# Optimization experiments

Hardware: AMD Instinct MI355X
Metric: run time of the kernel (lower is better)

## Reference

```python
import jax, jax.numpy as jnp
import numpy as np

B, NQ, NM, NHR, D, H, FF = 16, 100, 5440, 4096, 256, 8, 2048

def _ln(x, w, b):
    m = x.mean(-1, keepdims=True)
    v = ((x - m) ** 2).mean(-1, keepdims=True)
    return (x - m) * jax.lax.rsqrt(v + 1e-5) * w + b

def setup_inputs():
    key = jax.random.key(0)
    ks = iter(jax.random.split(key, 32))
    def rn(shape, s=1.0):
        return jax.random.normal(next(ks), shape, jnp.float32) * s
    return {
        'tgt': rn((B, NQ, D)),
        'memory': rn((B, NM, D)),
        'memory_hr': rn((B, NHR, D)),
        'prior_attn_bias': rn((B, NQ, NM)),
        'query_pos': rn((B, NQ, D)),
        'ln_cross_w': jnp.ones((D,)), 'ln_cross_b': jnp.zeros((D,)),
        'q_w': rn((D, D), 0.02), 'q_b': jnp.zeros((D,)),
        'k_w': rn((D, D), 0.02), 'k_b': jnp.zeros((D,)),
        'v_w': rn((D, D), 0.02), 'v_b': jnp.zeros((D,)),
        'out_w': rn((D, D), 0.02), 'out_b': jnp.zeros((D,)),
        'ln_self_w': jnp.ones((D,)), 'ln_self_b': jnp.zeros((D,)),
        'sa_in_w': rn((3 * D, D), 0.02), 'sa_in_b': jnp.zeros((3 * D,)),
        'sa_out_w': rn((D, D), 0.02), 'sa_out_b': jnp.zeros((D,)),
        'ln_ffn_w': jnp.ones((D,)), 'ln_ffn_b': jnp.zeros((D,)),
        'lin1_w': rn((FF, D), 0.02), 'lin1_b': jnp.zeros((FF,)),
        'lin2_w': rn((D, FF), 0.02), 'lin2_b': jnp.zeros((D,)),
        'me_w': rn((D, D), 0.02), 'me_b': jnp.zeros((D,)),
    }

def reference(tgt, memory, memory_hr, prior_attn_bias, query_pos,
              ln_cross_w, ln_cross_b, q_w, q_b, k_w, k_b, v_w, v_b,
              out_w, out_b, ln_self_w, ln_self_b, sa_in_w, sa_in_b,
              sa_out_w, sa_out_b, ln_ffn_w, ln_ffn_b, lin1_w, lin1_b,
              lin2_w, lin2_b, me_w, me_b):
    b, nq, d = tgt.shape
    nm = memory.shape[1]
    h = H
    dh = d // h
    scale = dh ** -0.5
    # ---- cross-attention with additive prior bias (eval mode: dropout = id) ----
    x = _ln(tgt, ln_cross_w, ln_cross_b)
    q = ((x + query_pos) @ q_w.T + q_b).reshape(b, nq, h, dh)
    k = (memory @ k_w.T + k_b).reshape(b, nm, h, dh)
    v = (memory @ v_w.T + v_b).reshape(b, nm, h, dh)
    attn = jnp.einsum('bqhd,bmhd->bhqm', q, k) * scale + prior_attn_bias[:, None]  # [b,h,nq,nm]
    a = jax.nn.softmax(attn, axis=-1)
    o = jnp.einsum('bhqm,bmhd->bqhd', a, v).reshape(b, nq, d)
    tgt = tgt + (o @ out_w.T + out_b)
    # ---- self-attention (torch nn.MultiheadAttention, batch_first, eval) ----
    z = _ln(tgt, ln_self_w, ln_self_b)
    zq = z + query_pos
    qs = (zq @ sa_in_w[:d].T + sa_in_b[:d]).reshape(b, nq, h, dh)
    ks = (zq @ sa_in_w[d:2 * d].T + sa_in_b[d:2 * d]).reshape(b, nq, h, dh)
    vs = (z @ sa_in_w[2 * d:].T + sa_in_b[2 * d:]).reshape(b, nq, h, dh)
    sattn = jax.nn.softmax(jnp.einsum('bqhd,bmhd->bhqm', qs, ks) * scale, axis=-1)
    so = jnp.einsum('bhqm,bmhd->bqhd', sattn, vs).reshape(b, nq, d)
    tgt = tgt + (so @ sa_out_w.T + sa_out_b)
    # ---- FFN ----
    y = _ln(tgt, ln_ffn_w, ln_ffn_b)
    y = jax.nn.gelu(y @ lin1_w.T + lin1_b, approximate=False) @ lin2_w.T + lin2_b
    tgt = tgt + y
    # ---- mask branch ----
    mask_logits = jnp.einsum('bqd,bmd->bqm', tgt @ me_w.T + me_b, memory_hr)
    return (tgt, mask_logits)
```

## Files before the change

kernel.cpp:

```cpp
#include <hip/hip_runtime.h>

typedef unsigned short u16;
typedef unsigned int u32;
typedef __bf16 bf16x8 __attribute__((ext_vector_type(8)));
typedef float f32x4 __attribute__((ext_vector_type(4)));
typedef float f32x16 __attribute__((ext_vector_type(16)));

#define NCH 34
#define NSTEP 5

__device__ __forceinline__ u16 f2b(float f) {
  u32 u = __float_as_uint(f);
  u32 r = (u + 0x7fffu + ((u >> 16) & 1u)) >> 16;
  return (u16)r;
}
__device__ __forceinline__ float b2f(u16 h) {
  return __uint_as_float(((u32)h) << 16);
}
__device__ __forceinline__ bf16x8 zero8() {
  union { uint4 u; bf16x8 v; } z; z.u = make_uint4(0u, 0u, 0u, 0u); return z.v;
}
__device__ __forceinline__ u32 cvtpk(float lo, float hi) {
  u32 r;
  asm("v_cvt_pk_bf16_f32 %0, %1, %2" : "=v"(r) : "v"(lo), "v"(hi));
  return r;
}

struct Seg { const float* in; u16* out; int n4; };
struct PrepArgs {
  Seg seg[7];
  const float *k_w, *v_w, *k_b, *v_b, *pbias;
  u16 *Wf;
  uint4 *biasT5;
  float *kvB;
};

__global__ __launch_bounds__(256)
void prep_kernel(PrepArgs a)
{
  __shared__ float S[100][34];
  const int bx = blockIdx.x, tid = threadIdx.x;
  if (bx < 1472) {
    int bxr = bx;
#pragma unroll
    for (int k = 0; k < 7; ++k) {
      const int nb = a.seg[k].n4 >> 8;
      if (bxr < nb) {
        const int i = bxr * 256 + tid;
        const float4 f = *(const float4*)(a.seg[k].in + (size_t)i * 4);
        uint2 pk; pk.x = cvtpk(f.x, f.y); pk.y = cvtpk(f.z, f.w);
        *(uint2*)(a.seg[k].out + (size_t)i * 4) = pk;
        return;
      }
      bxr -= nb;
    }
    return;
  } else if (bx < 1536) {
    const int i = bx - 1472, gI = i >> 3, ks = i & 7;
    const int nt = tid >> 6, lane = tid & 63, lr = lane & 15, g = lane >> 4;
    const float* src = (gI < 4 ? a.k_w + (size_t)(gI * 64 + nt * 16 + lr) * 256
                               : a.v_w + (size_t)((gI - 4) * 64 + nt * 16 + lr) * 256)
                       + ks * 32 + g * 8;
    const float4 f0 = *(const float4*)src;
    const float4 f1 = *(const float4*)(src + 4);
    uint4 pk;
    pk.x = cvtpk(f0.x, f0.y); pk.y = cvtpk(f0.z, f0.w);
    pk.z = cvtpk(f1.x, f1.y); pk.w = cvtpk(f1.z, f1.w);
    *(uint4*)(a.Wf + (size_t)((gI * 8 + ks) * 4 + nt) * 512 + lane * 8) = pk;
  } else if (bx < 1538) {
    const int i = (bx - 1536) * 256 + tid;
    a.kvB[i] = (i < 256) ? a.k_b[i] : a.v_b[i - 256];
  } else {
    const int bt = bx - 1538;
    const int b = bt / 170, sg = bt - b * 170;
    const int m0 = sg * 32;
    for (int idx = tid; idx < 800; idx += 256) {
      const int q = idx >> 3, seg = idx & 7;
      const float4 v = *(const float4*)(a.pbias + (size_t)(b * 100 + q) * 5440 + m0 + seg * 4);
      S[q][seg * 4 + 0] = v.x; S[q][seg * 4 + 1] = v.y;
      S[q][seg * 4 + 2] = v.z; S[q][seg * 4 + 3] = v.w;
    }
    __syncthreads();
#pragma unroll
    for (int pass = 0; pass < 2; ++pass) {
      const int idx = pass * 256 + tid;
      const int qb = idx >> 7, r2 = idx & 127;
      const int half = r2 >> 6, lane = r2 & 63;
      const int q = qb * 32 + (lane & 31), hh = lane >> 5;
      u16 hv[8];
#pragma unroll
      for (int i = 0; i < 8; ++i) {
        const int reg = half * 8 + i;
        const int m = (reg & 3) + 8 * (reg >> 2) + 4 * hh;
        hv[i] = (q < 100) ? f2b(S[q][m]) : (u16)0;
      }
      uint4 pk;
      pk.x = (u32)hv[0] | ((u32)hv[1] << 16);
      pk.y = (u32)hv[2] | ((u32)hv[3] << 16);
      pk.z = (u32)hv[4] | ((u32)hv[5] << 16);
      pk.w = (u32)hv[6] | ((u32)hv[7] << 16);
      a.biasT5[((size_t)(bt * 4 + qb)) * 128 + half * 64 + lane] = pk;
    }
  }
}

template<int ROWS>
__device__ __forceinline__ void ln_stage(const float* __restrict__ x, int row0,
    const float* __restrict__ w, const float* __restrict__ b,
    const float* __restrict__ pos, u16* As)
{
  const int tid = threadIdx.x, lane = tid & 63, wid = tid >> 6;
  const float4 wv = *(const float4*)(w + lane * 4);
  const float4 bv = *(const float4*)(b + lane * 4);
#pragma unroll
  for (int rr = 0; rr < ROWS / 4; ++rr) {
    const int rl = wid * (ROWS / 4) + rr;
    const size_t o = (size_t)(row0 + rl) * 256 + lane * 4;
    const float4 v = *(const float4*)(x + o);
    float s = v.x + v.y + v.z + v.w;
#pragma unroll
    for (int m = 1; m < 64; m <<= 1) s += __shfl_xor(s, m);
    const float mean = s * (1.f / 256.f);
    const float d0 = v.x - mean, d1 = v.y - mean, d2 = v.z - mean, d3 = v.w - mean;
    float ss = d0 * d0 + d1 * d1 + d2 * d2 + d3 * d3;
#pragma unroll
    for (int m = 1; m < 64; m <<= 1) ss += __shfl_xor(ss, m);
    const float rs = rsqrtf(ss * (1.f / 256.f) + 1e-5f);
    float y0 = d0 * rs * wv.x + bv.x;
    float y1 = d1 * rs * wv.y + bv.y;
    float y2 = d2 * rs * wv.z + bv.z;
    float y3 = d3 * rs * wv.w + bv.w;
    if (pos) {
      const float4 pv = *(const float4*)(pos + o);
      y0 += pv.x; y1 += pv.y; y2 += pv.z; y3 += pv.w;
    }
    uint2 pk; pk.x = cvtpk(y0, y1); pk.y = cvtpk(y2, y3);
    const int byte = (rl * 512 + lane * 8) ^ ((rl & 7) << 4);
    *(uint2*)((char*)As + byte) = pk;
  }
}

__device__ __forceinline__ void gemm16x128(const u16* As, const u16* __restrict__ W,
                                           u16 (*Ws)[40], f32x4 acc[2])
{
  const int tid = threadIdx.x, lane = tid & 63, wid = tid >> 6;
  const int g = lane >> 4, lr = lane & 15;
  for (int k0 = 0; k0 < 256; k0 += 32) {
    for (int cid = tid; cid < 512; cid += 256) {
      const int r = cid >> 2, cg = (cid & 3) * 8;
      *(uint4*)&Ws[r][cg] = *(const uint4*)(W + (size_t)r * 256 + k0 + cg);
    }
    __syncthreads();
    const int abyte = (lr * 512 + k0 * 2 + g * 16) ^ ((lr & 7) << 4);
    const bf16x8 af = *(const bf16x8*)((const char*)As + abyte);
#pragma unroll
    for (int nt = 0; nt < 2; ++nt) {
      const bf16x8 bfr = *(const bf16x8*)&Ws[wid * 32 + nt * 16 + lr][g * 8];
      acc[nt] = __builtin_amdgcn_mfma_f32_16x16x32_bf16(af, bfr, acc[nt], 0, 0, 0);
    }
    __syncthreads();
  }
}

__global__ __launch_bounds__(256)
void qproj_kernel(const float* __restrict__ x, const float* __restrict__ lnw,
                  const float* __restrict__ lnb, const float* __restrict__ pos,
                  const u16* __restrict__ W, const float* __restrict__ bias,
                  u16* __restrict__ out, float scale)
{
  __shared__ u16 As[16 * 256];
  __shared__ u16 Ws[128][40];
  const int tid = threadIdx.x, lane = tid & 63, wid = tid >> 6;
  const int g = lane >> 4, lr = lane & 15;
  const int row0 = blockIdx.x * 16, n0 = blockIdx.y * 128;
  ln_stage<16>(x, row0, lnw, lnb, pos, As);
  f32x4 acc[2] = {};
  gemm16x128(As, W + (size_t)n0 * 256, Ws, acc);
#pragma unroll
  for (int nt = 0; nt < 2; ++nt) {
    const int col = n0 + wid * 32 + nt * 16 + lr;
    const float bv = bias[col];
#pragma unroll
    for (int r = 0; r < 4; ++r) {
      const int row = row0 + g * 4 + r;
      out[(size_t)row * 256 + col] = f2b((acc[nt][r] + bv) * scale);
    }
  }
}

__global__ __launch_bounds__(256)
void sain_kernel(const float* __restrict__ x, const float* __restrict__ lnw,
                 const float* __restrict__ lnb, const float* __restrict__ pos,
                 const u16* __restrict__ W, const float* __restrict__ bias,
                 float* __restrict__ qkb, float* __restrict__ vsb)
{
  __shared__ u16 As[16 * 256];
  __shared__ u16 Ws[128][40];
  const int tid = threadIdx.x, lane = tid & 63, wid = tid >> 6;
  const int g = lane >> 4, lr = lane & 15;
  const int row0 = blockIdx.x * 16, y = blockIdx.y;
  ln_stage<16>(x, row0, lnw, lnb, (y < 4) ? pos : nullptr, As);
  f32x4 acc[2] = {};
  gemm16x128(As, W + (size_t)y * 128 * 256, Ws, acc);
#pragma unroll
  for (int nt = 0; nt < 2; ++nt) {
    const int cl = wid * 32 + nt * 16 + lr;
    const float bv = bias[y * 128 + cl];
#pragma unroll
    for (int r = 0; r < 4; ++r) {
      const int row = row0 + g * 4 + r;
      const float v = acc[nt][r] + bv;
      if (y < 4) qkb[(size_t)row * 512 + y * 128 + cl] = v;
      else       vsb[(size_t)row * 256 + (y - 4) * 128 + cl] = v;
    }
  }
}

__global__ __launch_bounds__(256)
void ffn1_kernel(const float* __restrict__ x, const float* __restrict__ lnw,
                 const float* __restrict__ lnb, const u16* __restrict__ W,
                 const float* __restrict__ bias, u16* __restrict__ out)
{
  __shared__ u16 As[64 * 256];
  __shared__ u16 Ws[256][40];
  const int tid = threadIdx.x, lane = tid & 63, wid = tid >> 6;
  const int g = lane >> 4, lr = lane & 15;
  const int row0 = blockIdx.x * 64, n0 = blockIdx.y * 256;
  ln_stage<64>(x, row0, lnw, lnb, nullptr, As);
  f32x4 acc[16] = {};
  for (int k0 = 0; k0 < 256; k0 += 32) {
    for (int cid = tid; cid < 1024; cid += 256) {
      const int r = cid >> 2, cg = (cid & 3) * 8;
      *(uint4*)&Ws[r][cg] = *(const uint4*)(W + (size_t)(n0 + r) * 256 + k0 + cg);
    }
    __syncthreads();
    const int arow = wid * 16 + lr;
    const int abyte = (arow * 512 + k0 * 2 + g * 16) ^ ((arow & 7) << 4);
    const bf16x8 af = *(const bf16x8*)((const char*)As + abyte);
#pragma unroll
    for (int nt = 0; nt < 16; ++nt) {
      const bf16x8 bfr = *(const bf16x8*)&Ws[nt * 16 + lr][g * 8];
      acc[nt] = __builtin_amdgcn_mfma_f32_16x16x32_bf16(af, bfr, acc[nt], 0, 0, 0);
    }
    __syncthreads();
  }
#pragma unroll
  for (int nt = 0; nt < 16; ++nt) {
    const int col = n0 + nt * 16 + lr;
    const float bv = bias[col];
#pragma unroll
    for (int r = 0; r < 4; ++r) {
      const int row = row0 + wid * 16 + g * 4 + r;
      float v = acc[nt][r] + bv;
      v = 0.5f * v * (1.f + erff(v * 0.70710678118654752f));
      out[(size_t)row * 2048 + col] = f2b(v);
    }
  }
}

template<int BM, int BN, int WM, int WN, int GELU_, int RES_, int OF32, int OBF>
__global__ __launch_bounds__(256)
void gemm_kernel(const u16* __restrict__ Ap, const u16* __restrict__ W,
                 const float* __restrict__ bias, const float* __restrict__ res,
                 float* __restrict__ Cf, u16* __restrict__ Cb,
                 int M, int N, int K, float scale)
{
  constexpr int WROWS = BM / WM;
  constexpr int WCOLS = BN / WN;
  constexpr int MT = WROWS / 16;
  constexpr int NT = WCOLS / 16;
  static_assert(WM * WN == 4, "4 waves");
  __shared__ u16 As[BM][40];
  __shared__ u16 Ws[BN][40];
  const int tid = threadIdx.x, lane = tid & 63, wid = tid >> 6;
  const int g = lane >> 4, lr = lane & 15;
  const int m0 = blockIdx.x * BM, n0 = blockIdx.y * BN;
  const int wm = wid / WN, wn = wid % WN;
  f32x4 acc[MT][NT] = {};
  for (int k0 = 0; k0 < K; k0 += 32) {
    for (int cid = tid; cid < BM * 4; cid += 256) {
      int r = cid >> 2, cg = (cid & 3) * 8;
      *(uint4*)&As[r][cg] = *(const uint4*)(Ap + (size_t)(m0 + r) * K + k0 + cg);
    }
    for (int cid = tid; cid < BN * 4; cid += 256) {
      int r = cid >> 2, cg = (cid & 3) * 8;
      *(uint4*)&Ws[r][cg] = *(const uint4*)(W + (size_t)(n0 + r) * K + k0 + cg);
    }
    __syncthreads();
    bf16x8 af[MT], bfr[NT];
#pragma unroll
    for (int mt = 0; mt < MT; ++mt) af[mt] = *(const bf16x8*)&As[wm * WROWS + mt * 16 + lr][g * 8];
#pragma unroll
    for (int nt = 0; nt < NT; ++nt) bfr[nt] = *(const bf16x8*)&Ws[wn * WCOLS + nt * 16 + lr][g * 8];
#pragma unroll
    for (int mt = 0; mt < MT; ++mt)
#pragma unroll
      for (int nt = 0; nt < NT; ++nt)
        acc[mt][nt] = __builtin_amdgcn_mfma_f32_16x16x32_bf16(af[mt], bfr[nt], acc[mt][nt], 0, 0, 0);
    __syncthreads();
  }
#pragma unroll
  for (int mt = 0; mt < MT; ++mt)
#pragma unroll
    for (int nt = 0; nt < NT; ++nt) {
      const int col = n0 + wn * WCOLS + nt * 16 + lr;
      const float bv = bias[col];
#pragma unroll
      for (int r = 0; r < 4; ++r) {
        const int row = m0 + wm * WROWS + mt * 16 + g * 4 + r;
        float v = (acc[mt][nt][r] + bv) * scale;
        if constexpr (GELU_) v = 0.5f * v * (1.f + erff(v * 0.70710678118654752f));
        if constexpr (RES_) v += res[(size_t)row * N + col];
        if constexpr (OF32) Cf[(size_t)row * N + col] = v;
        if constexpr (OBF) Cb[(size_t)row * N + col] = f2b(v);
      }
    }
}

__global__ __launch_bounds__(512, 4)
void kv_gemm_kernel(const float* __restrict__ A, const u16* __restrict__ Wf,
                    const float* __restrict__ biasKV,
                    u16* __restrict__ Kb, u16* __restrict__ Vt)
{
  __shared__ u16 As[64 * 256];
  __shared__ u16 Vs[256 * 64];
  const int tid = threadIdx.x, lane = tid & 63, wid = tid >> 6;
  const int g = lane >> 4, lr = lane & 15;
  const int bidx = blockIdx.x / 85, t = blockIdx.x - bidx * 85;
  const int row0 = blockIdx.x * 64;

  for (int ch = tid; ch < 2048; ch += 512) {
    const int r = ch >> 5, c8 = (ch & 31) * 8;
    const float* ap = A + (size_t)(row0 + r) * 256 + c8;
    const float4 f0 = *(const float4*)ap;
    const float4 f1 = *(const float4*)(ap + 4);
    uint4 pk;
    pk.x = cvtpk(f0.x, f0.y);
    pk.y = cvtpk(f0.z, f0.w);
    pk.z = cvtpk(f1.x, f1.y);
    pk.w = cvtpk(f1.z, f1.w);
    const int byte = r * 512 + c8 * 2;
    *(uint4*)((char*)As + (byte ^ ((r & 7) << 4))) = pk;
  }
  __syncthreads();

  const u16* wbase = Wf + (size_t)wid * 8 * 4 * 512 + lane * 8;
  f32x4 acc[4][4] = {};
#pragma unroll 2
  for (int ks = 0; ks < 8; ++ks) {
    bf16x8 bfv[4], af[4];
#pragma unroll
    for (int nt = 0; nt < 4; ++nt)
      bfv[nt] = *(const bf16x8*)(wbase + (ks * 4 + nt) * 512);
#pragma unroll
    for (int mt = 0; mt < 4; ++mt) {
      const int r = mt * 16 + lr;
      const int byte = r * 512 + ks * 64 + g * 16;
      af[mt] = *(const bf16x8*)((const char*)As + (byte ^ ((r & 7) << 4)));
    }
#pragma unroll
    for (int mt = 0; mt < 4; ++mt)
#pragma unroll
      for (int nt = 0; nt < 4; ++nt)
        acc[mt][nt] = __builtin_amdgcn_mfma_f32_16x16x32_bf16(af[mt], bfv[nt], acc[mt][nt], 0, 0, 0);
  }

  const int isV = wid >> 2;
  if (isV) {
#pragma unroll
    for (int nt = 0; nt < 4; ++nt) {
      const int col = (wid - 4) * 64 + nt * 16 + lr;
      const float bv = biasKV[256 + col];
#pragma unroll
      for (int mt = 0; mt < 4; ++mt) {
        const int slot = (mt >> 1) * 32 + 16 * (mt & 1) + 8 * (g & 1) + 4 * (g >> 1);
#pragma unroll
        for (int r = 0; r < 4; r += 2) {
          const u32 val = cvtpk(acc[mt][nt][r] + bv, acc[mt][nt][r + 1] + bv);
          const int byte = (col * 128 + (slot + r) * 2) ^ ((col & 7) << 4);
          *(u32*)((char*)Vs + byte) = val;
        }
      }
    }
  }
  __syncthreads();

  if (!isV) {
#pragma unroll
    for (int nt = 0; nt < 4; ++nt) {
      const int col = wid * 64 + nt * 16 + lr;
      const float bv = biasKV[col];
#pragma unroll
      for (int mt = 0; mt < 4; ++mt)
#pragma unroll
        for (int r = 0; r < 4; r += 2) {
          const u32 pk = cvtpk(acc[mt][nt][r] + bv, acc[mt][nt][r + 1] + bv);
          const int rowA = mt * 16 + g * 4 + r;
          const int rowB = rowA + 1;
          *(u16*)((char*)As + ((rowA * 512 + col * 2) ^ ((rowA & 7) << 4))) = (u16)pk;
          *(u16*)((char*)As + ((rowB * 512 + col * 2) ^ ((rowB & 7) << 4))) = (u16)(pk >> 16);
        }
    }
  } else {
    const size_t vbase = (size_t)bidx * 256 * 5440 + (size_t)t * 64;
    const int t2 = tid - 256;
#pragma unroll
    for (int p = 0; p < 8; ++p) {
      const int idx = p * 256 + t2;
      const int col = idx >> 3, chunk = idx & 7;
      const int lbyte = col * 128 + ((chunk * 16) ^ ((col & 7) << 4));
      const uint4 v = *(const uint4*)((const char*)Vs + lbyte);
      *(uint4*)(Vt + vbase + (size_t)col * 5440 + chunk * 8) = v;
    }
  }
  __syncthreads();
#pragma unroll
  for (int p = 0; p < 4; ++p) {
    const int idx = p * 512 + tid;
    const int row = idx >> 5, c16 = idx & 31;
    const int lbyte = row * 512 + ((c16 * 16) ^ ((row & 7) << 4));
    const uint4 v = *(const uint4*)((const char*)As + lbyte);
    *(uint4*)(Kb + (size_t)(row0 + row) * 256 + c16 * 8) = v;
  }
}

__global__ __launch_bounds__(256, 3)
void cross_attn_kernel(const u16* __restrict__ Q, const u16* __restrict__ Kb,
                       const u16* __restrict__ Vt, const uint4* __restrict__ biasT5,
                       u32* __restrict__ Opp, float* __restrict__ ML)
{
  const int tid = threadIdx.x, lane = tid & 63, wid = tid >> 6;
  const int ql = lane & 31, hh = lane >> 5;
  const int b = blockIdx.y, c = blockIdx.x;
  const int head = blockIdx.z * 4 + wid;
  const int m_base = c * (5440 / NCH);

  bf16x8 qf[4][2];
#pragma unroll
  for (int qb = 0; qb < 4; ++qb) {
    const int q = qb * 32 + ql;
#pragma unroll
    for (int hf = 0; hf < 2; ++hf)
      qf[qb][hf] = (q < 100)
        ? *(const bf16x8*)&Q[(size_t)(b * 100 + q) * 256 + head * 32 + hf * 16 + hh * 8]
        : zero8();
  }
  float M[4], L[4];
  f32x16 O[4];
#pragma unroll
  for (int qb = 0; qb < 4; ++qb) {
    M[qb] = -1e30f; L[qb] = 0.f;
#pragma unroll
    for (int i = 0; i < 16; ++i) O[qb][i] = 0.f;
  }

  for (int s = 0; s < NSTEP; ++s) {
    const int m0 = m_base + s * 32;
    const u16* kp = &Kb[(size_t)(b * 5440 + m0 + ql) * 256 + head * 32 + hh * 8];
    const bf16x8 kf0 = *(const bf16x8*)kp;
    const bf16x8 kf1 = *(const bf16x8*)(kp + 16);
    const u16* vp = &Vt[((size_t)(b * 8 + head) * 32 + ql) * 5440 + m0 + hh * 8];
    const bf16x8 vf0 = *(const bf16x8*)vp;
    const bf16x8 vf1 = *(const bf16x8*)(vp + 16);
    const uint4* bb = biasT5 + ((size_t)(b * 170 + c * NSTEP + s) * 4) * 128 + lane;
#pragma unroll
    for (int qb = 0; qb < 4; ++qb) {
      const uint4 b0 = bb[qb * 128];
      const uint4 b1 = bb[qb * 128 + 64];
      f32x16 Sv = {};
      __builtin_amdgcn_s_setprio(1);
      Sv = __builtin_amdgcn_mfma_f32_32x32x16_bf16(kf0, qf[qb][0], Sv, 0, 0, 0);
      Sv = __builtin_amdgcn_mfma_f32_32x32x16_bf16(kf1, qf[qb][1], Sv, 0, 0, 0);
      __builtin_amdgcn_s_setprio(0);
      const u32 bw[8] = {b0.x, b0.y, b0.z, b0.w, b1.x, b1.y, b1.z, b1.w};
#pragma unroll
      for (int i = 0; i < 8; ++i) {
        Sv[2 * i]     += b2f((u16)bw[i]);
        Sv[2 * i + 1] += b2f((u16)(bw[i] >> 16));
      }
      float t8[8];
#pragma unroll
      for (int i = 0; i < 8; ++i) t8[i] = fmaxf(Sv[2 * i], Sv[2 * i + 1]);
      float t4a = fmaxf(fmaxf(t8[0], t8[1]), fmaxf(t8[2], t8[3]));
      float t4b = fmaxf(fmaxf(t8[4], t8[5]), fmaxf(t8[6], t8[7]));
      float mx = fmaxf(t4a, t4b);
      mx = fmaxf(mx, __shfl_xor(mx, 32));
      const float newM = fmaxf(M[qb], mx);
      const float al = __expf(M[qb] - newM);
      M[qb] = newM;
      float p[16];
#pragma unroll
      for (int i = 0; i < 16; ++i) p[i] = __expf(Sv[i] - newM);
      float s8[8];
#pragma unroll
      for (int i = 0; i < 8; ++i) s8[i] = p[2 * i] + p[2 * i + 1];
      const float sum = ((s8[0] + s8[1]) + (s8[2] + s8[3])) + ((s8[4] + s8[5]) + (s8[6] + s8[7]));
      L[qb] = L[qb] * al + sum;
#pragma unroll
      for (int i = 0; i < 16; ++i) O[qb][i] *= al;
      union { uint4 u; bf16x8 v; } pb0, pb1;
      pb0.u.x = cvtpk(p[0], p[1]);   pb0.u.y = cvtpk(p[2], p[3]);
      pb0.u.z = cvtpk(p[4], p[5]);   pb0.u.w = cvtpk(p[6], p[7]);
      pb1.u.x = cvtpk(p[8], p[9]);   pb1.u.y = cvtpk(p[10], p[11]);
      pb1.u.z = cvtpk(p[12], p[13]); pb1.u.w = cvtpk(p[14], p[15]);
      __builtin_amdgcn_s_setprio(1);
      O[qb] = __builtin_amdgcn_mfma_f32_32x32x16_bf16(vf0, pb0.v, O[qb], 0, 0, 0);
      O[qb] = __builtin_amdgcn_mfma_f32_32x32x16_bf16(vf1, pb1.v, O[qb], 0, 0, 0);
      __builtin_amdgcn_s_setprio(0);
    }
  }
  const int bh = b * 8 + head;
#pragma unroll
  for (int qb = 0; qb < 4; ++qb) {
    const int q = qb * 32 + ql;
    const float Lt = L[qb] + __shfl_xor(L[qb], 32);
    if (q < 100) {
      const size_t rb = (size_t)(bh * NCH + c) * 128 + q;
#pragma unroll
      for (int i = 0; i < 8; ++i)
        Opp[rb * 16 + hh * 8 + i] = cvtpk(O[qb][2 * i], O[qb][2 * i + 1]);
      if (hh == 0) { ML[rb * 2] = M[qb]; ML[rb * 2 + 1] = Lt; }
    }
  }
}

__global__ __launch_bounds__(256)
void reduce_attn_kernel(const u32* __restrict__ Opp, const float* __restrict__ ML,
                        u16* __restrict__ outb)
{
  const int row = blockIdx.x;
  const int b = row / 100, q = row % 100;
  const int h = threadIdx.x >> 5, d = threadIdx.x & 31;
  const int bh = b * 8 + h;
  const int reg = (d & 3) + 4 * (d >> 3);
  const int slot = ((d >> 2) & 1) * 8 + (reg >> 1);
  const int half = reg & 1;
  float gm = -1e30f;
  for (int c = 0; c < NCH; ++c) gm = fmaxf(gm, ML[((size_t)(bh * NCH + c) * 128 + q) * 2]);
  float l = 0.f, o = 0.f;
  for (int c = 0; c < NCH; ++c) {
    const size_t rb = (size_t)(bh * NCH + c) * 128 + q;
    const float w = __expf(ML[rb * 2] - gm);
    l += ML[rb * 2 + 1] * w;
    const u32 pv = Opp[rb * 16 + slot];
    o += b2f((u16)(half ? (pv >> 16) : pv)) * w;
  }
  outb[(size_t)row * 256 + h * 32 + d] = f2b(o / l);
}

__global__ __launch_bounds__(128)
void self_attn_kernel(const float* __restrict__ qk, const float* __restrict__ vs,
                      u16* __restrict__ so)
{
  __shared__ u16 kk[100][36];
  __shared__ u16 vv[100][36];
  __shared__ float S[100][101];
  const int b = blockIdx.x >> 3, h = blockIdx.x & 7;
  const int t = threadIdx.x;
  for (int e = t; e < 3200; e += 128) {
    const int r = e >> 5, cq = e & 31;
    kk[r][cq] = f2b(qk[(size_t)(b * 100 + r) * 512 + 256 + h * 32 + cq]);
    vv[r][cq] = f2b(vs[(size_t)(b * 100 + r) * 256 + h * 32 + cq]);
  }
  __syncthreads();
  if (t < 100) {
    float qr_[32];
#pragma unroll
    for (int cq = 0; cq < 32; ++cq) qr_[cq] = qk[(size_t)(b * 100 + t) * 512 + h * 32 + cq];
    for (int m = 0; m < 100; ++m) {
      float dp = 0.f;
#pragma unroll
      for (int cq = 0; cq < 32; ++cq) dp += qr_[cq] * b2f(kk[m][cq]);
      S[t][m] = dp * 0.17677669529663687f;
    }
    float mx = -1e30f;
    for (int m = 0; m < 100; ++m) mx = fmaxf(mx, S[t][m]);
    float sum = 0.f;
    for (int m = 0; m < 100; ++m) { const float p = __expf(S[t][m] - mx); S[t][m] = p; sum += p; }
    const float inv = 1.f / sum;
    float o[32];
#pragma unroll
    for (int cq = 0; cq < 32; ++cq) o[cq] = 0.f;
    for (int m = 0; m < 100; ++m) {
      const float p = S[t][m];
#pragma unroll
      for (int cq = 0; cq < 32; ++cq) o[cq] += p * b2f(vv[m][cq]);
    }
#pragma unroll
    for (int cq = 0; cq < 32; ++cq)
      so[(size_t)(b * 100 + t) * 256 + h * 32 + cq] = f2b(o[cq] * inv);
  }
}

__global__ __launch_bounds__(256)
void mask_gemm_kernel(const u16* __restrict__ tm, const float* __restrict__ hr,
                      float* __restrict__ out)
{
  __shared__ u16 As[112][40];
  __shared__ u16 Bs[64][40];
  const int tid = threadIdx.x, lane = tid & 63, wid = tid >> 6;
  const int g = lane >> 4, lr = lane & 15;
  const int b = blockIdx.y, n0 = blockIdx.x * 64;
  f32x4 acc[7] = {};
  for (int k0 = 0; k0 < 256; k0 += 32) {
    for (int cid = tid; cid < 448; cid += 256) {
      const int r = cid >> 2, cg = (cid & 3) * 8;
      uint4 val = {0u, 0u, 0u, 0u};
      if (r < 100) val = *(const uint4*)&tm[(size_t)(b * 100 + r) * 256 + k0 + cg];
      *(uint4*)&As[r][cg] = val;
    }
    {
      const int r = tid >> 2, cg = (tid & 3) * 8;
      const float* hp = hr + (size_t)(b * 4096 + n0 + r) * 256 + k0 + cg;
      float4 f0 = *(const float4*)hp;
      float4 f1 = *(const float4*)(hp + 4);
      uint4 pk;
      pk.x = cvtpk(f0.x, f0.y); pk.y = cvtpk(f0.z, f0.w);
      pk.z = cvtpk(f1.x, f1.y); pk.w = cvtpk(f1.z, f1.w);
      *(uint4*)&Bs[r][cg] = pk;
    }
    __syncthreads();
    const bf16x8 bfr = *(const bf16x8*)&Bs[wid * 16 + lr][g * 8];
#pragma unroll
    for (int mt = 0; mt < 7; ++mt) {
      const bf16x8 af = *(const bf16x8*)&As[mt * 16 + lr][g * 8];
      acc[mt] = __builtin_amdgcn_mfma_f32_16x16x32_bf16(af, bfr, acc[mt], 0, 0, 0);
    }
    __syncthreads();
  }
#pragma unroll
  for (int mt = 0; mt < 7; ++mt)
#pragma unroll
    for (int r = 0; r < 4; ++r) {
      const int qr = mt * 16 + g * 4 + r;
      if (qr < 100)
        out[(size_t)(b * 100 + qr) * 4096 + n0 + wid * 16 + lr] = acc[mt][r];
    }
}

extern "C" void kernel_launch(void* const* d_in, const int* in_sizes, int n_in,
                              void* d_out, int out_size, void* d_ws, size_t ws_size,
                              hipStream_t stream)
{
  (void)in_sizes; (void)n_in; (void)out_size; (void)ws_size;
  const float* tgt      = (const float*)d_in[0];
  const float* memory   = (const float*)d_in[1];
  const float* memhr    = (const float*)d_in[2];
  const float* pbias    = (const float*)d_in[3];
  const float* qpos     = (const float*)d_in[4];
  const float* lncw     = (const float*)d_in[5];
  const float* lncb     = (const float*)d_in[6];
  const float* q_w      = (const float*)d_in[7];
  const float* q_b      = (const float*)d_in[8];
  const float* k_w      = (const float*)d_in[9];
  const float* k_b      = (const float*)d_in[10];
  const float* v_w      = (const float*)d_in[11];
  const float* v_b      = (const float*)d_in[12];
  const float* out_w    = (const float*)d_in[13];
  const float* out_b    = (const float*)d_in[14];
  const float* lnsw     = (const float*)d_in[15];
  const float* lnsb     = (const float*)d_in[16];
  const float* sa_in_w  = (const float*)d_in[17];
  const float* sa_in_b  = (const float*)d_in[18];
  const float* sa_out_w = (const float*)d_in[19];
  const float* sa_out_b = (const float*)d_in[20];
  const float* lnfw     = (const float*)d_in[21];
  const float* lnfb     = (const float*)d_in[22];
  const float* l1w      = (const float*)d_in[23];
  const float* l1b      = (const float*)d_in[24];
  const float* l2w      = (const float*)d_in[25];
  const float* l2b      = (const float*)d_in[26];
  const float* me_w     = (const float*)d_in[27];
  const float* me_b     = (const float*)d_in[28];
  float* outf = (float*)d_out;

  char* ws = (char*)d_ws;
  size_t off = 0;
  auto alloc = [&](size_t bytes) -> void* {
    void* p = ws + off;
    off = (off + bytes + 255) & ~(size_t)255;
    return p;
  };
  u16*   Wf    = (u16*)alloc((size_t)131072 * 2);
  u16*   qW    = (u16*)alloc((size_t)65536 * 2);
  u16*   outW  = (u16*)alloc((size_t)65536 * 2);
  u16*   saW   = (u16*)alloc((size_t)196608 * 2);
  u16*   saoW  = (u16*)alloc((size_t)65536 * 2);
  u16*   l1W   = (u16*)alloc((size_t)524288 * 2);
  u16*   l2W   = (u16*)alloc((size_t)524288 * 2);
  u16*   meW   = (u16*)alloc((size_t)65536 * 2);
  float* kvB   = (float*)alloc((size_t)512 * 4);
  uint4* biasT5= (uint4*)alloc((size_t)16 * 170 * 4 * 128 * 16);
  u16*   Qb    = (u16*)alloc((size_t)409600 * 2);
  u16*   Kb    = (u16*)alloc((size_t)22282240 * 2);
  u16*   Vt    = (u16*)alloc((size_t)22282240 * 2);
  u32*   Opp   = (u32*)alloc((size_t)(128 * NCH * 128 * 16) * 4);
  float* MLp   = (float*)alloc((size_t)(128 * NCH * 128 * 2) * 4);
  u16*   attno = (u16*)alloc((size_t)409600 * 2);
  float* tgt1  = (float*)alloc((size_t)409600 * 4);
  float* qkb   = (float*)alloc((size_t)819200 * 4);
  float* vsb   = (float*)alloc((size_t)409600 * 4);
  u16*   sob   = (u16*)alloc((size_t)409600 * 2);
  float* tgt2  = (float*)alloc((size_t)409600 * 4);
  u16*   hb    = (u16*)alloc((size_t)3276800 * 2);
  u16*   t3b   = (u16*)alloc((size_t)409600 * 2);
  u16*   tmb   = (u16*)alloc((size_t)409600 * 2);

  const float SCALE = 0.17677669529663687f;

  PrepArgs pa;
  pa.seg[0] = {q_w,      qW,   16384};
  pa.seg[1] = {out_w,    outW, 16384};
  pa.seg[2] = {sa_in_w,  saW,  49152};
  pa.seg[3] = {sa_out_w, saoW, 16384};
  pa.seg[4] = {l1w,      l1W,  131072};
  pa.seg[5] = {l2w,      l2W,  131072};
  pa.seg[6] = {me_w,     meW,  16384};
  pa.k_w = k_w; pa.v_w = v_w; pa.k_b = k_b; pa.v_b = v_b; pa.pbias = pbias;
  pa.Wf = Wf; pa.biasT5 = biasT5; pa.kvB = kvB;
  prep_kernel<<<4258, 256, 0, stream>>>(pa);

  qproj_kernel<<<dim3(100, 2), 256, 0, stream>>>(tgt, lncw, lncb, qpos, qW, q_b, Qb, SCALE);
  kv_gemm_kernel<<<dim3(1360), 512, 0, stream>>>(memory, Wf, kvB, Kb, Vt);
  cross_attn_kernel<<<dim3(NCH, 16, 2), 256, 0, stream>>>(Qb, Kb, Vt, biasT5, Opp, MLp);
  reduce_attn_kernel<<<1600, 256, 0, stream>>>(Opp, MLp, attno);
  gemm_kernel<16, 128, 1, 4, 0, 1, 1, 0><<<dim3(100, 2), 256, 0, stream>>>(
      attno, outW, out_b, tgt, tgt1, nullptr, 1600, 256, 256, 1.f);

  sain_kernel<<<dim3(100, 6), 256, 0, stream>>>(tgt1, lnsw, lnsb, qpos, saW, sa_in_b, qkb, vsb);
  self_attn_kernel<<<128, 128, 0, stream>>>(qkb, vsb, sob);
  gemm_kernel<16, 128, 1, 4, 0, 1, 1, 0><<<dim3(100, 2), 256, 0, stream>>>(
      sob, saoW, sa_out_b, tgt1, tgt2, nullptr, 1600, 256, 256, 1.f);

  ffn1_kernel<<<dim3(25, 8), 256, 0, stream>>>(tgt2, lnfw, lnfb, l1W, l1b, hb);
  gemm_kernel<16, 128, 1, 4, 0, 1, 1, 1><<<dim3(100, 2), 256, 0, stream>>>(
      hb, l2W, l2b, tgt2, outf, t3b, 1600, 256, 2048, 1.f);

  gemm_kernel<16, 128, 1, 4, 0, 0, 0, 1><<<dim3(100, 2), 256, 0, stream>>>(
      t3b, meW, me_b, nullptr, nullptr, tmb, 1600, 256, 256, 1.f);
  mask_gemm_kernel<<<dim3(64, 16), 256, 0, stream>>>(tmb, memhr, outf + 409600);
}
```

Before: 336.7 us.

## Use base-2 softmax, lazy max rescaling, and prefetch K/V in cross-attention

Folds log2(e) into the query scale and the prepacked bias so the cross-attention softmax can use exp2 directly instead of __expf. The online-softmax rescale of O and L is skipped unless some lane's running max grows by more than 8 (in log2 units), which removes most of the per-step rescale multiplies. K/V fragments for the next step are loaded one iteration ahead to overlap global loads with MFMA and softmax work. The lazy-rescale threshold allows probabilities up to 2^8 before renormalisation, which could affect bf16 precision of P.

```diff
diff --git a/kernel.cpp b/kernel.cpp
--- a/kernel.cpp
+++ b/kernel.cpp
@@ -8,6 +8,7 @@
 
 #define NCH 34
 #define NSTEP 5
+#define LOG2E 1.4426950408889634f
 
 __device__ __forceinline__ u16 f2b(float f) {
   u32 u = __float_as_uint(f);
@@ -92,7 +93,7 @@
       for (int i = 0; i < 8; ++i) {
         const int reg = half * 8 + i;
         const int m = (reg & 3) + 8 * (reg >> 2) + 4 * hh;
-        hv[i] = (q < 100) ? f2b(S[q][m]) : (u16)0;
+        hv[i] = (q < 100) ? f2b(S[q][m] * LOG2E) : (u16)0;
       }
       uint4 pk;
       pk.x = (u32)hv[0] | ((u32)hv[1] << 16);
@@ -454,14 +455,23 @@
     for (int i = 0; i < 16; ++i) O[qb][i] = 0.f;
   }
 
+  const u16* kbase = &Kb[(size_t)(b * 5440 + m_base + ql) * 256 + head * 32 + hh * 8];
+  const u16* vbase = &Vt[((size_t)(b * 8 + head) * 32 + ql) * 5440 + m_base + hh * 8];
+  bf16x8 kf0 = *(const bf16x8*)kbase;
+  bf16x8 kf1 = *(const bf16x8*)(kbase + 16);
+  bf16x8 vf0 = *(const bf16x8*)vbase;
+  bf16x8 vf1 = *(const bf16x8*)(vbase + 16);
+
   for (int s = 0; s < NSTEP; ++s) {
-    const int m0 = m_base + s * 32;
-    const u16* kp = &Kb[(size_t)(b * 5440 + m0 + ql) * 256 + head * 32 + hh * 8];
-    const bf16x8 kf0 = *(const bf16x8*)kp;
-    const bf16x8 kf1 = *(const bf16x8*)(kp + 16);
-    const u16* vp = &Vt[((size_t)(b * 8 + head) * 32 + ql) * 5440 + m0 + hh * 8];
-    const bf16x8 vf0 = *(const bf16x8*)vp;
-    const bf16x8 vf1 = *(const bf16x8*)(vp + 16);
+    bf16x8 nk0 = kf0, nk1 = kf1, nv0 = vf0, nv1 = vf1;
+    if (s + 1 < NSTEP) {
+      const u16* kp = kbase + (size_t)(s + 1) * 32 * 256;
+      const u16* vp = vbase + (s + 1) * 32;
+      nk0 = *(const bf16x8*)kp;
+      nk1 = *(const bf16x8*)(kp + 16);
+      nv0 = *(const bf16x8*)vp;
+      nv1 = *(const bf16x8*)(vp + 16);
+    }
     const uint4* bb = biasT5 + ((size_t)(b * 170 + c * NSTEP + s) * 4) * 128 + lane;
 #pragma unroll
     for (int qb = 0; qb < 4; ++qb) {
@@ -485,19 +495,21 @@
       float t4b = fmaxf(fmaxf(t8[4], t8[5]), fmaxf(t8[6], t8[7]));
       float mx = fmaxf(t4a, t4b);
       mx = fmaxf(mx, __shfl_xor(mx, 32));
-      const float newM = fmaxf(M[qb], mx);
-      const float al = __expf(M[qb] - newM);
-      M[qb] = newM;
+      if (!__all(mx - M[qb] <= 8.f)) {
+        const float newM = fmaxf(M[qb], mx);
+        const float al = exp2f(M[qb] - newM);
+        M[qb] = newM;
+        L[qb] *= al;
+#pragma unroll
+        for (int i = 0; i < 16; ++i) O[qb][i] *= al;
+      }
       float p[16];
 #pragma unroll
-      for (int i = 0; i < 16; ++i) p[i] = __expf(Sv[i] - newM);
+      for (int i = 0; i < 16; ++i) p[i] = exp2f(Sv[i] - M[qb]);
       float s8[8];
 #pragma unroll
       for (int i = 0; i < 8; ++i) s8[i] = p[2 * i] + p[2 * i + 1];
-      const float sum = ((s8[0] + s8[1]) + (s8[2] + s8[3])) + ((s8[4] + s8[5]) + (s8[6] + s8[7]));
-      L[qb] = L[qb] * al + sum;
-#pragma unroll
-      for (int i = 0; i < 16; ++i) O[qb][i] *= al;
+      L[qb] += ((s8[0] + s8[1]) + (s8[2] + s8[3])) + ((s8[4] + s8[5]) + (s8[6] + s8[7]));
       union { uint4 u; bf16x8 v; } pb0, pb1;
       pb0.u.x = cvtpk(p[0], p[1]);   pb0.u.y = cvtpk(p[2], p[3]);
       pb0.u.z = cvtpk(p[4], p[5]);   pb0.u.w = cvtpk(p[6], p[7]);
@@ -508,6 +520,7 @@
       O[qb] = __builtin_amdgcn_mfma_f32_32x32x16_bf16(vf1, pb1.v, O[qb], 0, 0, 0);
       __builtin_amdgcn_s_setprio(0);
     }
+    kf0 = nk0; kf1 = nk1; vf0 = nv0; vf1 = nv1;
   }
   const int bh = b * 8 + head;
 #pragma unroll
@@ -540,7 +553,7 @@
   float l = 0.f, o = 0.f;
   for (int c = 0; c < NCH; ++c) {
     const size_t rb = (size_t)(bh * NCH + c) * 128 + q;
-    const float w = __expf(ML[rb * 2] - gm);
+    const float w = exp2f(ML[rb * 2] - gm);
     l += ML[rb * 2 + 1] * w;
     const u32 pv = Opp[rb * 16 + slot];
     o += b2f((u16)(half ? (pv >> 16) : pv)) * w;
@@ -706,7 +719,7 @@
   u16*   t3b   = (u16*)alloc((size_t)409600 * 2);
   u16*   tmb   = (u16*)alloc((size_t)409600 * 2);
 
-  const float SCALE = 0.17677669529663687f;
+  const float SCALE = 0.17677669529663687f * LOG2E;
 
   PrepArgs pa;
   pa.seg[0] = {q_w,      qW,   16384};
```

Result: slower. 389.4 us (+15.6%).
